# Optimization experiments

Hardware: AMD Instinct MI355X
Metric: run time of the kernel (lower is better)

The kernel has to match this reference:

```python
import jax, jax.numpy as jnp
import numpy as np

QDIM = 1024; KDIM = 2048; NH = 16; HD = QDIM // NH
H = 64; W = 64; B = 8; S2 = 256
EPS = 1e-6; SCALE = HD ** -0.5


def setup_inputs() -> dict:
    key = jax.random.key(0)
    ks = jax.random.split(key, 8)
    def lin(k, fan_in, shape):
        lim = 1.0 / np.sqrt(fan_in)
        return jax.random.uniform(k, shape, jnp.float32, -lim, lim)
    return {
        "x": jax.random.normal(ks[0], (B, H * W, QDIM), jnp.float32),
        "y": jax.random.normal(ks[1], (B, S2, KDIM), jnp.float32),
        "wq": lin(ks[2], QDIM, (QDIM, QDIM)),
        "bq": lin(ks[3], QDIM, (QDIM,)),
        "wkv": lin(ks[4], KDIM, (2 * QDIM, KDIM)),
        "bkv": lin(ks[5], KDIM, (2 * QDIM,)),
        "wo": lin(ks[6], QDIM, (QDIM, QDIM)),
        "bo": lin(ks[7], QDIM, (QDIM,)),
        "qn_g": jnp.ones((HD,), jnp.float32),
        "qn_b": jnp.zeros((HD,), jnp.float32),
        "kn_g": jnp.ones((HD,), jnp.float32),
        "kn_b": jnp.zeros((HD,), jnp.float32),
    }


def _layernorm(t, g, b):
    mu = t.mean(-1, keepdims=True)
    var = ((t - mu) ** 2).mean(-1, keepdims=True)
    return (t - mu) * jax.lax.rsqrt(var + EPS) * g + b


def _rope_2d_angles():
    # Lumina-style 2D rotary: head_dim//2 complex freqs per position,
    # interleaving H-axis and W-axis frequencies along the pair dim.
    d4 = HD // 4
    inv = 1.0 / (10000.0 ** (np.arange(0, HD // 2, 2, dtype=np.float32) / (HD // 2)))  # (d4,)
    fh = np.outer(np.arange(H, dtype=np.float32), inv)  # (H, d4)
    fw = np.outer(np.arange(W, dtype=np.float32), inv)  # (W, d4)
    ang = np.stack([
        np.broadcast_to(fh[:, None, :], (H, W, d4)),
        np.broadcast_to(fw[None, :, :], (H, W, d4)),
    ], axis=-1).reshape(H, W, HD // 2)  # interleaved h,w,h,w,...
    return jnp.asarray(np.cos(ang)), jnp.asarray(np.sin(ang))


def reference(x, y, wq, bq, wkv, bkv, wo, bo, qn_g, qn_b, kn_g, kn_b):
    b, s1, c = x.shape
    q = (x @ wq.T + bq).reshape(b, s1, NH, HD).transpose(0, 2, 1, 3)          # (b, nh, s1, hd)
    kv = (y @ wkv.T + bkv).reshape(b, -1, 2, NH, HD).transpose(0, 2, 3, 1, 4)  # (b, 2, nh, s2, hd)
    k, v = kv[:, 0], kv[:, 1]
    q = _layernorm(q, qn_g, qn_b)
    k = _layernorm(k, kn_g, kn_b)
    # inline 2D RoPE on Q only (complex mult on interleaved pairs)
    cos, sin = _rope_2d_angles()                                               # (H, W, hd//2)
    qr = q.reshape(b, NH, H, W, HD // 2, 2)
    qe, qo = qr[..., 0], qr[..., 1]
    q = jnp.stack([qe * cos - qo * sin, qe * sin + qo * cos], axis=-1).reshape(b, NH, s1, HD)
    attn = jax.nn.softmax((q * SCALE) @ jnp.swapaxes(k, -2, -1), axis=-1)      # (b, nh, s1, s2)
    out = (attn @ v).transpose(0, 2, 1, 3).reshape(b, s1, c)
    return out @ wo.T + bo
```

## Files before the change

kernel.cpp:

```cpp
#include <hip/hip_runtime.h>
#include <hip/hip_bf16.h>

typedef __bf16 bf16x8 __attribute__((ext_vector_type(8)));
typedef __bf16 bf16x4 __attribute__((ext_vector_type(4)));
typedef float f32x4 __attribute__((ext_vector_type(4)));

__device__ __forceinline__ void async_copy16(__bf16* lds_base, const __bf16* g) {
  __builtin_amdgcn_global_load_lds(
      (const __attribute__((address_space(1))) void*)g,
      (__attribute__((address_space(3))) void*)lds_base, 16, 0, 0);
}

__global__ __launch_bounds__(256) void cvt_bf16(const float* __restrict__ in,
                                                __bf16* __restrict__ out, int n4) {
  int i = blockIdx.x * 256 + threadIdx.x;
  if (i >= n4) return;
  float4 v = ((const float4*)in)[i];
  bf16x4 o;
  o.x = (__bf16)v.x; o.y = (__bf16)v.y; o.z = (__bf16)v.z; o.w = (__bf16)v.w;
  ((bf16x4*)out)[i] = o;
}

template<bool STORE_BF16>
__global__ __launch_bounds__(256) void gemm_bt(const __bf16* __restrict__ A,
                                               const __bf16* __restrict__ Bw,
                                               const float* __restrict__ bias,
                                               void* __restrict__ Cp,
                                               int M, int N, int K) {
  __shared__ __align__(16) __bf16 sA[128 * 64];
  __shared__ __align__(16) __bf16 sB[128 * 64];
  const int tid = threadIdx.x;
  const int lane = tid & 63;
  const int w = tid >> 6;
  const int wr = w >> 1, wc = w & 1;
  const int l15 = lane & 15, q4 = lane >> 4;
  const int bm = blockIdx.x, bn = blockIdx.y;

  f32x4 acc[4][4] = {};

  for (int k0 = 0; k0 < K; k0 += 64) {
    __syncthreads();
#pragma unroll
    for (int it = 0; it < 4; ++it) {
      int chunk = it * 256 + tid;
      int row = chunk >> 3, c8 = chunk & 7;
      int ldsbase = (it * 256 + w * 64) * 8;
      async_copy16(sA + ldsbase, A + (size_t)(bm * 128 + row) * K + k0 + c8 * 8);
      async_copy16(sB + ldsbase, Bw + (size_t)(bn * 128 + row) * K + k0 + c8 * 8);
    }
    __syncthreads();
#pragma unroll
    for (int kk = 0; kk < 2; ++kk) {
      bf16x8 af[4], bfr[4];
#pragma unroll
      for (int i = 0; i < 4; ++i)
        af[i] = *(const bf16x8*)(sA + (wr * 64 + i * 16 + l15) * 64 + kk * 32 + q4 * 8);
#pragma unroll
      for (int j = 0; j < 4; ++j)
        bfr[j] = *(const bf16x8*)(sB + (wc * 64 + j * 16 + l15) * 64 + kk * 32 + q4 * 8);
#pragma unroll
      for (int i = 0; i < 4; ++i)
#pragma unroll
        for (int j = 0; j < 4; ++j)
          acc[i][j] = __builtin_amdgcn_mfma_f32_16x16x32_bf16(af[i], bfr[j], acc[i][j], 0, 0, 0);
    }
  }
#pragma unroll
  for (int j = 0; j < 4; ++j) {
    const int col = bn * 128 + wc * 64 + j * 16 + l15;
    const float bv = bias[col];
#pragma unroll
    for (int i = 0; i < 4; ++i) {
      const int row0 = bm * 128 + wr * 64 + i * 16 + q4 * 4;
#pragma unroll
      for (int r = 0; r < 4; ++r) {
        float v = acc[i][j][r] + bv;
        size_t off = (size_t)(row0 + r) * N + col;
        if (STORE_BF16) ((__bf16*)Cp)[off] = (__bf16)v;
        else            ((float*)Cp)[off]  = v;
      }
    }
  }
}

__global__ __launch_bounds__(256) void kv_epilogue(const float* __restrict__ kv,
                                                   const float* __restrict__ g,
                                                   const float* __restrict__ bta,
                                                   __bf16* __restrict__ Kd,
                                                   __bf16* __restrict__ VT) {
  const int lane = threadIdx.x & 63;
  const int vec = blockIdx.x * 4 + (threadIdx.x >> 6);
  const int nh = vec & 15;
  const int sv = (vec >> 4) & 1;
  const int row = vec >> 5;
  const int b = row >> 8, s2 = row & 255;
  float v = kv[(size_t)row * 2048 + sv * 1024 + nh * 64 + lane];
  if (sv == 0) {
    float mu = v;
#pragma unroll
    for (int o = 32; o; o >>= 1) mu += __shfl_xor(mu, o);
    mu *= (1.f / 64.f);
    float d = v - mu;
    float va = d * d;
#pragma unroll
    for (int o = 32; o; o >>= 1) va += __shfl_xor(va, o);
    va *= (1.f / 64.f);
    float xn = d * rsqrtf(va + 1e-6f) * g[lane] + bta[lane];
    Kd[(((size_t)b * 16 + nh) * 256 + s2) * 64 + lane] = (__bf16)xn;
  } else {
    VT[(((size_t)b * 16 + nh) * 64 + lane) * 256 + s2] = (__bf16)v;
  }
}

__global__ __launch_bounds__(256) void q_epilogue(const __bf16* __restrict__ qraw,
                                                  const float* __restrict__ g,
                                                  const float* __restrict__ bta,
                                                  __bf16* __restrict__ Q) {
  const int lane = threadIdx.x & 63;
  const int vec = blockIdx.x * 4 + (threadIdx.x >> 6);
  const int nh = vec & 15;
  const int row = vec >> 4;
  float v = (float)qraw[(size_t)row * 1024 + nh * 64 + lane];
  float mu = v;
#pragma unroll
  for (int o = 32; o; o >>= 1) mu += __shfl_xor(mu, o);
  mu *= (1.f / 64.f);
  float d = v - mu;
  float va = d * d;
#pragma unroll
  for (int o = 32; o; o >>= 1) va += __shfl_xor(va, o);
  va *= (1.f / 64.f);
  float xn = d * rsqrtf(va + 1e-6f) * g[lane] + bta[lane];
  const int s1 = row & 4095;
  const int hh = s1 >> 6, wpix = s1 & 63;
  const int t = lane >> 2;
  const int usew = (lane >> 1) & 1;
  float inv = __expf(-(float)t * 0.5756462732485114f);
  float ang = (usew ? (float)wpix : (float)hh) * inv;
  float cc = __cosf(ang), ssn = __sinf(ang);
  float partner = __shfl_xor(xn, 1);
  float rot = xn * cc + partner * ssn * ((lane & 1) ? 1.f : -1.f);
  rot *= 0.125f;
  const int b = row >> 12;
  Q[(((size_t)b * 16 + nh) * 4096 + (size_t)s1) * 64 + lane] = (__bf16)rot;
}

__global__ __launch_bounds__(256) void attn_kernel(const __bf16* __restrict__ Q,
                                                   const __bf16* __restrict__ Kd,
                                                   const __bf16* __restrict__ VT,
                                                   __bf16* __restrict__ O) {
  __shared__ __align__(16) __bf16 sK[256 * 64];
  __shared__ __align__(16) __bf16 sV[64 * 256];
  const int tid = threadIdx.x, lane = tid & 63, w = tid >> 6;
  const int l15 = lane & 15, q4 = lane >> 4;
  const int s7 = l15 & 7;
  const int bh = blockIdx.y;
  const int m0 = blockIdx.x * 64;
  const __bf16* Kg = Kd + (size_t)bh * 256 * 64;
  const __bf16* Vg = VT + (size_t)bh * 64 * 256;
  const __bf16* Qg = Q + ((size_t)bh * 4096 + m0) * 64;
#pragma unroll
  for (int it = 0; it < 8; ++it) {
    int c = it * 256 + tid;
    int kr = c >> 3, kh = c & 7;
    *(uint4*)(sK + kr * 64 + ((kh ^ (kr & 7)) * 8)) = *(const uint4*)(Kg + c * 8);
    int vr = c >> 5, vh = c & 31;
    *(uint4*)(sV + vr * 256 + ((vh ^ (vr & 7)) * 8)) = *(const uint4*)(Vg + c * 8);
  }
  bf16x8 qf0 = *(const bf16x8*)(Qg + (w * 16 + l15) * 64 + q4 * 8);
  bf16x8 qf1 = *(const bf16x8*)(Qg + (w * 16 + l15) * 64 + 32 + q4 * 8);
  __syncthreads();
  f32x4 sacc[16] = {};
#pragma unroll
  for (int mt = 0; mt < 16; ++mt) {
    bf16x8 a0 = *(const bf16x8*)(sK + (mt * 16 + l15) * 64 + ((q4 ^ s7) * 8));
    bf16x8 a1 = *(const bf16x8*)(sK + (mt * 16 + l15) * 64 + (((4 + q4) ^ s7) * 8));
    sacc[mt] = __builtin_amdgcn_mfma_f32_16x16x32_bf16(a0, qf0, sacc[mt], 0, 0, 0);
    sacc[mt] = __builtin_amdgcn_mfma_f32_16x16x32_bf16(a1, qf1, sacc[mt], 0, 0, 0);
  }
  __syncthreads();
  float mx = -1e30f;
#pragma unroll
  for (int mt = 0; mt < 16; ++mt)
#pragma unroll
    for (int r = 0; r < 4; ++r) mx = fmaxf(mx, sacc[mt][r]);
  mx = fmaxf(mx, __shfl_xor(mx, 16));
  mx = fmaxf(mx, __shfl_xor(mx, 32));
  float l = 0.f;
#pragma unroll
  for (int mt = 0; mt < 16; ++mt)
#pragma unroll
    for (int r = 0; r < 4; ++r) {
      float p = __expf(sacc[mt][r] - mx);
      sacc[mt][r] = p;
      l += p;
    }
  l += __shfl_xor(l, 16);
  l += __shfl_xor(l, 32);
  const float linv = 1.f / l;
#pragma unroll
  for (int mt = 0; mt < 16; ++mt) {
    bf16x4 pk;
    pk.x = (__bf16)(sacc[mt][0] * linv);
    pk.y = (__bf16)(sacc[mt][1] * linv);
    pk.z = (__bf16)(sacc[mt][2] * linv);
    pk.w = (__bf16)(sacc[mt][3] * linv);
    int chunk = mt * 2 + (q4 >> 1);
    *(bf16x4*)(sK + (w * 16 + l15) * 256 + ((chunk ^ s7) * 8) + (q4 & 1) * 4) = pk;
  }
  f32x4 oacc[4] = {};
#pragma unroll
  for (int ks = 0; ks < 8; ++ks) {
    int phys = ((ks * 4 + q4) ^ s7) * 8;
    bf16x8 a = *(const bf16x8*)(sK + (w * 16 + l15) * 256 + phys);
#pragma unroll
    for (int j = 0; j < 4; ++j) {
      bf16x8 b = *(const bf16x8*)(sV + (j * 16 + l15) * 256 + phys);
      oacc[j] = __builtin_amdgcn_mfma_f32_16x16x32_bf16(a, b, oacc[j], 0, 0, 0);
    }
  }
  const int b = bh >> 4, nh = bh & 15;
#pragma unroll
  for (int j = 0; j < 4; ++j)
#pragma unroll
    for (int r = 0; r < 4; ++r) {
      size_t off = ((size_t)b * 4096 + m0 + w * 16 + q4 * 4 + r) * 1024
                 + nh * 64 + j * 16 + l15;
      O[off] = (__bf16)oacc[j][r];
    }
}

extern "C" void kernel_launch(void* const* d_in, const int* in_sizes, int n_in,
                              void* d_out, int out_size, void* d_ws, size_t ws_size,
                              hipStream_t stream) {
  const float* x    = (const float*)d_in[0];
  const float* y    = (const float*)d_in[1];
  const float* wq   = (const float*)d_in[2];
  const float* bq   = (const float*)d_in[3];
  const float* wkv  = (const float*)d_in[4];
  const float* bkv  = (const float*)d_in[5];
  const float* wo   = (const float*)d_in[6];
  const float* bo   = (const float*)d_in[7];
  const float* qng  = (const float*)d_in[8];
  const float* qnb  = (const float*)d_in[9];
  const float* kng  = (const float*)d_in[10];
  const float* knb  = (const float*)d_in[11];
  float* out = (float*)d_out;

  char* ws = (char*)d_ws;
  size_t off = 0;
  auto take = [&](size_t bytes) { char* p = ws + off; off += (bytes + 255) & ~(size_t)255; return p; };
  __bf16* xb   = (__bf16*)take((size_t)32768 * 1024 * 2);
  char*  reg1  = take((size_t)32768 * 1024 * 2);
  __bf16* Qb   = (__bf16*)take((size_t)32768 * 1024 * 2);
  __bf16* yb   = (__bf16*)take((size_t)2048 * 2048 * 2);
  __bf16* wqb  = (__bf16*)take((size_t)1024 * 1024 * 2);
  __bf16* wkvb = (__bf16*)take((size_t)2048 * 2048 * 2);
  __bf16* wob  = (__bf16*)take((size_t)1024 * 1024 * 2);
  __bf16* Kb   = (__bf16*)take((size_t)128 * 256 * 64 * 2);
  __bf16* VTb  = (__bf16*)take((size_t)128 * 64 * 256 * 2);
  float*  kvf  = (float*)reg1;
  __bf16* qraw = (__bf16*)reg1;
  __bf16* aout = xb;

  cvt_bf16<<<32768, 256, 0, stream>>>(x,   xb,   8388608);
  cvt_bf16<<<4096,  256, 0, stream>>>(y,   yb,   1048576);
  cvt_bf16<<<1024,  256, 0, stream>>>(wq,  wqb,  262144);
  cvt_bf16<<<4096,  256, 0, stream>>>(wkv, wkvb, 1048576);
  cvt_bf16<<<1024,  256, 0, stream>>>(wo,  wob,  262144);

  gemm_bt<false><<<dim3(16, 16), 256, 0, stream>>>(yb, wkvb, bkv, kvf, 2048, 2048, 2048);
  kv_epilogue<<<16384, 256, 0, stream>>>(kvf, kng, knb, Kb, VTb);

  gemm_bt<true><<<dim3(256, 8), 256, 0, stream>>>(xb, wqb, bq, qraw, 32768, 1024, 1024);
  q_epilogue<<<131072, 256, 0, stream>>>(qraw, qng, qnb, Qb);

  attn_kernel<<<dim3(64, 128), 256, 0, stream>>>(Qb, Kb, VTb, aout);

  gemm_bt<false><<<dim3(256, 8), 256, 0, stream>>>(aout, wob, bo, out, 32768, 1024, 1024);
}
```

Measured before the change: 712.9 us.

## Add 256x256-tile GEMM with 4-stage async LDS pipeline for Q and output projections

Adds a 512-thread GEMM kernel that computes 256x256 output tiles per block. It streams A and B through a four-deep ring of LDS buffers using direct global-to-LDS async loads, with swizzled addressing to avoid bank conflicts. MFMA work is split into two half-steps interleaved with the prefetches and wave priority bumps. The Q and output projections switch to it, aiming for more reuse per loaded byte and better overlap of loads with math, at the cost of high register and LDS pressure.

```diff
diff --git a/kernel.cpp b/kernel.cpp
--- a/kernel.cpp
+++ b/kernel.cpp
@@ -75,6 +75,123 @@
 #pragma unroll
       for (int r = 0; r < 4; ++r) {
         float v = acc[i][j][r] + bv;
+        size_t off = (size_t)(row0 + r) * N + col;
+        if (STORE_BF16) ((__bf16*)Cp)[off] = (__bf16)v;
+        else            ((float*)Cp)[off]  = v;
+      }
+    }
+  }
+}
+
+template<int KK, bool STORE_BF16>
+__global__ __launch_bounds__(512, 2) void gemm_bt_big(const __bf16* __restrict__ A,
+                                                      const __bf16* __restrict__ Bw,
+                                                      const float* __restrict__ bias,
+                                                      void* __restrict__ Cp,
+                                                      int N) {
+  static_assert(KK % 32 == 0 && KK / 32 >= 4, "KK");
+  constexpr int NT = KK / 32;
+  __shared__ __align__(16) __bf16 sA[4 * 256 * 32];
+  __shared__ __align__(16) __bf16 sB[4 * 256 * 32];
+  const int tid = threadIdx.x;
+  const int lane = tid & 63;
+  const int w = tid >> 6;
+  const int wr = w >> 2, wc = w & 3;
+  const int l15 = lane & 15, q4 = lane >> 4;
+  const int bm = blockIdx.x, bn = blockIdx.y;
+
+  const int r0 = tid >> 2;
+  const int csw = (tid & 3) ^ (r0 & 3);
+  const __bf16* gA0 = A + (size_t)(bm * 256 + r0) * KK + csw * 8;
+  const __bf16* gA1 = gA0 + (size_t)128 * KK;
+  const __bf16* gB0 = Bw + (size_t)(bn * 256 + r0) * KK + csw * 8;
+  const __bf16* gB1 = gB0 + (size_t)128 * KK;
+  const int lds_w0 = (w * 64) * 8;
+  const int lds_w1 = (512 + w * 64) * 8;
+
+  const int qsw = (q4 ^ (l15 & 3)) * 8;
+  const int aBase = (wr * 128 + l15) * 32 + qsw;
+  const int bBase = (wc * 64 + l15) * 32 + qsw;
+
+  f32x4 acc[8][4] = {};
+
+#pragma unroll
+  for (int t = 0; t < 3; ++t) {
+    async_copy16(sA + t * 8192 + lds_w0, gA0 + t * 32);
+    async_copy16(sA + t * 8192 + lds_w1, gA1 + t * 32);
+    async_copy16(sB + t * 8192 + lds_w0, gB0 + t * 32);
+    async_copy16(sB + t * 8192 + lds_w1, gB1 + t * 32);
+  }
+  asm volatile("s_waitcnt vmcnt(8)" ::: "memory");
+  __builtin_amdgcn_s_barrier();
+  __builtin_amdgcn_sched_barrier(0);
+
+#pragma unroll 4
+  for (int t = 0; t < NT; ++t) {
+    const __bf16* sAs = sA + (t & 3) * 8192;
+    const __bf16* sBs = sB + (t & 3) * 8192;
+    const int ps = (t + 3) & 3;
+    const bool pf = (t + 3) < NT;
+
+    bf16x8 af[4], bfrag[4];
+#pragma unroll
+    for (int m = 0; m < 4; ++m)
+      af[m] = *(const bf16x8*)(sAs + aBase + m * 512);
+#pragma unroll
+    for (int n = 0; n < 4; ++n)
+      bfrag[n] = *(const bf16x8*)(sBs + bBase + n * 512);
+    if (pf) {
+      async_copy16(sA + ps * 8192 + lds_w0, gA0 + (t + 3) * 32);
+      async_copy16(sA + ps * 8192 + lds_w1, gA1 + (t + 3) * 32);
+    }
+    __builtin_amdgcn_s_barrier();
+    asm volatile("s_waitcnt lgkmcnt(0)" ::: "memory");
+    __builtin_amdgcn_sched_barrier(0);
+    __builtin_amdgcn_s_setprio(1);
+#pragma unroll
+    for (int m = 0; m < 4; ++m)
+#pragma unroll
+      for (int n = 0; n < 4; ++n)
+        acc[m][n] = __builtin_amdgcn_mfma_f32_16x16x32_bf16(af[m], bfrag[n], acc[m][n], 0, 0, 0);
+    __builtin_amdgcn_s_setprio(0);
+    __builtin_amdgcn_s_barrier();
+    __builtin_amdgcn_sched_barrier(0);
+
+    bf16x8 ag[4];
+#pragma unroll
+    for (int m = 0; m < 4; ++m)
+      ag[m] = *(const bf16x8*)(sAs + aBase + 2048 + m * 512);
+    if (pf) {
+      async_copy16(sB + ps * 8192 + lds_w0, gB0 + (t + 3) * 32);
+      async_copy16(sB + ps * 8192 + lds_w1, gB1 + (t + 3) * 32);
+    }
+    if (pf)                 asm volatile("s_waitcnt vmcnt(8)" ::: "memory");
+    else if (t + 3 == NT)   asm volatile("s_waitcnt vmcnt(4)" ::: "memory");
+    else if (t + 2 == NT)   asm volatile("s_waitcnt vmcnt(0)" ::: "memory");
+    __builtin_amdgcn_s_barrier();
+    asm volatile("s_waitcnt lgkmcnt(0)" ::: "memory");
+    __builtin_amdgcn_sched_barrier(0);
+    __builtin_amdgcn_s_setprio(1);
+#pragma unroll
+    for (int m = 0; m < 4; ++m)
+#pragma unroll
+      for (int n = 0; n < 4; ++n)
+        acc[4 + m][n] = __builtin_amdgcn_mfma_f32_16x16x32_bf16(ag[m], bfrag[n], acc[4 + m][n], 0, 0, 0);
+    __builtin_amdgcn_s_setprio(0);
+    __builtin_amdgcn_s_barrier();
+    __builtin_amdgcn_sched_barrier(0);
+  }
+
+#pragma unroll
+  for (int n = 0; n < 4; ++n) {
+    const int col = bn * 256 + wc * 64 + n * 16 + l15;
+    const float bv = bias[col];
+#pragma unroll
+    for (int m = 0; m < 8; ++m) {
+      const int row0 = bm * 256 + wr * 128 + m * 16 + q4 * 4;
+#pragma unroll
+      for (int r = 0; r < 4; ++r) {
+        float v = acc[m][n][r] + bv;
         size_t off = (size_t)(row0 + r) * N + col;
         if (STORE_BF16) ((__bf16*)Cp)[off] = (__bf16)v;
         else            ((float*)Cp)[off]  = v;
@@ -272,10 +389,10 @@
   gemm_bt<false><<<dim3(16, 16), 256, 0, stream>>>(yb, wkvb, bkv, kvf, 2048, 2048, 2048);
   kv_epilogue<<<16384, 256, 0, stream>>>(kvf, kng, knb, Kb, VTb);
 
-  gemm_bt<true><<<dim3(256, 8), 256, 0, stream>>>(xb, wqb, bq, qraw, 32768, 1024, 1024);
+  gemm_bt_big<1024, true><<<dim3(128, 4), 512, 0, stream>>>(xb, wqb, bq, qraw, 1024);
   q_epilogue<<<131072, 256, 0, stream>>>(qraw, qng, qnb, Qb);
 
   attn_kernel<<<dim3(64, 128), 256, 0, stream>>>(Qb, Kb, VTb, aout);
 
-  gemm_bt<false><<<dim3(256, 8), 256, 0, stream>>>(aout, wob, bo, out, 32768, 1024, 1024);
-}
+  gemm_bt_big<1024, false><<<dim3(128, 4), 512, 0, stream>>>(aout, wob, bo, out, 1024);
+}
```

After: 681.6 us. -4.4%, faster.
